# Optimization experiments

Hardware: AMD Instinct MI355X
Metric: run time of the kernel (lower is better)

The kernel has to match this reference:

```python
import jax, jax.numpy as jnp
import numpy as np

E = 8       # num experts
T = 1024    # num tokens
H = 1024    # hidden dim
I = 1024    # intermediate dim (per gate/up half)


def setup_inputs() -> dict:
    key = jax.random.key(0)
    k1, k2, k3, k4 = jax.random.split(key, 4)
    return {
        "hidden_states": jax.random.normal(k1, (T, H), jnp.float32),
        "router_logits": jax.random.normal(k2, (T, E), jnp.float32),
        # W13 stored pre-transposed as in the module: [E, H, 2*I]
        "W13": jax.random.normal(k3, (E, H, 2 * I), jnp.float32) * 0.02,
        # W2 stored pre-transposed: [E, I, H]
        "W2": jax.random.normal(k4, (E, I, H), jnp.float32) * 0.02,
        "top_k": 2,
    }


def reference(hidden_states, router_logits, W13, W2, top_k):
    num_experts = router_logits.shape[-1]
    # --- routing: topk_softmax (softmax over all experts, then top-k) ---
    probs = jax.nn.softmax(router_logits, axis=-1)            # [T, E]
    w, idx = jax.lax.top_k(probs, top_k)                      # [T, K]
    # renormalize=True path of moe_gather
    w = w / jnp.sum(w, axis=-1, keepdims=True)
    # combine weights per expert: [T, E]
    combine = jnp.sum(jax.nn.one_hot(idx, num_experts, dtype=w.dtype) * w[..., None], axis=1)
    # --- grouped gate-up GEMM + silu_and_mul ---
    h13 = jnp.einsum('th,ehf->tef', hidden_states, W13)       # [T, E, 2I]
    gate, up = jnp.split(h13, 2, axis=-1)                     # each [T, E, I]
    act = jax.nn.silu(gate) * up                              # silu_and_mul
    # --- grouped down GEMM ---
    down = jnp.einsum('tei,eih->teh', act, W2)                # [T, E, H]
    # --- combine (moe_gather) ---
    return jnp.einsum('te,teh->th', combine, down)            # [T, H]
```

## Files before the change

### kernel.cpp

```cpp
#include <hip/hip_runtime.h>
#include <hip/hip_bf16.h>
#include <stdint.h>

#define NE    8
#define NTOK  1024
#define NH    1024
#define NI    1024
#define N13   2048
#define NPAIR 2048

#define P0_ITEMS 7169
#define G1MAX    736
#define G2MAX    624

typedef __attribute__((ext_vector_type(8))) short short8;
typedef __attribute__((ext_vector_type(4))) float f32x4;
typedef unsigned short u16;
typedef unsigned int   u32;

__device__ __forceinline__ u16 f2bf(float x) {
    union { float f; u32 u; } v; v.f = x;
    return (u16)((v.u + 0x7fffu + ((v.u >> 16) & 1u)) >> 16);
}

__device__ __forceinline__ void async_ld16(u16* lds, const u16* g) {
    __builtin_amdgcn_global_load_lds(
        (const __attribute__((address_space(1))) u32*)g,
        (__attribute__((address_space(3))) u32*)lds, 16, 0, 0);
}

__device__ __forceinline__ bool find_tile(
    const int* __restrict__ counts, int tile, int bm, int ntn,
    int& e_o, int& mt_o, int& nt_o, int& cnt_o, int& base_o)
{
    int base = 0;
    #pragma unroll
    for (int e = 0; e < NE; e++) {
        const int cnt = counts[e];
        const int mtiles = (cnt + bm - 1) / bm;
        const int tiles = mtiles * ntn;
        if (tile < tiles) {
            e_o = e; mt_o = tile / ntn; nt_o = tile - (tile / ntn) * ntn;
            cnt_o = cnt; base_o = base; return true;
        }
        tile -= tiles; base += cnt;
    }
    return false;
}

__global__ __launch_bounds__(256) void prep_all_kernel(
    const float* __restrict__ X, const float* __restrict__ logits,
    const float* __restrict__ W13, const float* __restrict__ W2,
    float* __restrict__ out, int* __restrict__ counts,
    int* __restrict__ pair_tok, float* __restrict__ pair_w,
    u16* __restrict__ Xb, u16* __restrict__ W13t, u16* __restrict__ W2t)
{
    __shared__ __align__(16) float Ts[64][65];
    const int tid = threadIdx.x;
    const int b = blockIdx.x;

    if (b == 0) {
        int* s_cnt  = (int*)&Ts[0][0];
        int* s_base = s_cnt + NE;
        if (tid < NE) s_cnt[tid] = 0;
        __syncthreads();
        int eA[4][2]; int slotA[4][2]; float wA[4][2];
        #pragma unroll
        for (int i = 0; i < 4; i++) {
            const int t = tid * 4 + i;
            float l[NE];
            #pragma unroll
            for (int e = 0; e < NE; e++) l[e] = logits[t * NE + e];
            int i0 = 0;
            #pragma unroll
            for (int e = 1; e < NE; e++) if (l[e] > l[i0]) i0 = e;
            int i1 = -1;
            #pragma unroll
            for (int e = 0; e < NE; e++) {
                if (e == i0) continue;
                if (i1 < 0 || l[e] > l[i1]) i1 = e;
            }
            const float e10 = __expf(l[i1] - l[i0]);
            const float inv = 1.0f / (1.0f + e10);
            eA[i][0] = i0; eA[i][1] = i1;
            wA[i][0] = inv; wA[i][1] = e10 * inv;
            slotA[i][0] = atomicAdd(&s_cnt[i0], 1);
            slotA[i][1] = atomicAdd(&s_cnt[i1], 1);
        }
        __syncthreads();
        if (tid == 0) {
            int acc = 0;
            #pragma unroll
            for (int e = 0; e < NE; e++) { s_base[e] = acc; acc += s_cnt[e]; }
        }
        __syncthreads();
        if (tid < NE) counts[tid] = s_cnt[tid];
        #pragma unroll
        for (int i = 0; i < 4; i++) {
            const int t = tid * 4 + i;
            #pragma unroll
            for (int k = 0; k < 2; k++) {
                const int p = s_base[eA[i][k]] + slotA[i][k];
                pair_tok[p] = t;
                pair_w[p]   = wA[i][k];
            }
        }
    } else if (b <= 512) {
        const int i = (b - 1) * 256 + tid;
        const float4* s = (const float4*)X;
        const float4 a = s[2 * i], c = s[2 * i + 1];
        uint4 o;
        o.x = f2bf(a.x) | ((u32)f2bf(a.y) << 16);
        o.y = f2bf(a.z) | ((u32)f2bf(a.w) << 16);
        o.z = f2bf(c.x) | ((u32)f2bf(c.y) << 16);
        o.w = f2bf(c.z) | ((u32)f2bf(c.w) << 16);
        *(uint4*)(Xb + (size_t)i * 8) = o;
    } else if (b <= 1024) {
        const int i = ((b - 513) * 256 + tid) * 8;
        const float4 z = make_float4(0.f, 0.f, 0.f, 0.f);
        *(float4*)(out + i)     = z;
        *(float4*)(out + i + 4) = z;
    } else {
        const int wb = b - 1025;
        const float* src; u16* dst; int K, N, tb;
        if (wb < 4096) { src = W13; dst = W13t; K = NH; N = N13; tb = wb; }
        else           { src = W2;  dst = W2t;  K = NI; N = NH;  tb = wb - 4096; }
        const int ktiles = K >> 6, ntiles = N >> 6;
        const int tpe = ktiles * ntiles;
        const int e = tb / tpe;
        const int rem = tb - e * tpe;
        const int kt = rem / ntiles, nt = rem - (rem / ntiles) * ntiles;
        const float* sb = src + ((size_t)e * K + (size_t)kt * 64) * N + nt * 64;
        #pragma unroll
        for (int i = 0; i < 4; i++) {
            const int idx = tid + i * 256;
            const int r = idx >> 4, c = (idx & 15) << 2;
            const float4 v = *(const float4*)(sb + (size_t)r * N + c);
            Ts[r][c + 0] = v.x; Ts[r][c + 1] = v.y;
            Ts[r][c + 2] = v.z; Ts[r][c + 3] = v.w;
        }
        __syncthreads();
        u16* db = dst + ((size_t)e * N + (size_t)nt * 64) * K + kt * 64;
        #pragma unroll
        for (int i = 0; i < 2; i++) {
            const int u = tid + i * 256;
            const int n = u >> 3, k8 = (u & 7) << 3;
            uint4 o;
            o.x = f2bf(Ts[k8 + 0][n]) | ((u32)f2bf(Ts[k8 + 1][n]) << 16);
            o.y = f2bf(Ts[k8 + 2][n]) | ((u32)f2bf(Ts[k8 + 3][n]) << 16);
            o.z = f2bf(Ts[k8 + 4][n]) | ((u32)f2bf(Ts[k8 + 5][n]) << 16);
            o.w = f2bf(Ts[k8 + 6][n]) | ((u32)f2bf(Ts[k8 + 7][n]) << 16);
            *(uint4*)(db + (size_t)n * K + k8) = o;
        }
    }
}

__global__ __launch_bounds__(256, 2) void gemm1_kernel(
    const u16* __restrict__ Xb, const u16* __restrict__ W13t,
    const int* __restrict__ counts, const int* __restrict__ pair_tok,
    u16* __restrict__ act)
{
    int e, mt, nt, cnt, base;
    if (!find_tile(counts, blockIdx.x, 128, NI / 32, e, mt, nt, cnt, base)) return;

    __shared__ u16 As[2][128 * 32];
    __shared__ u16 Bs[2][64 * 32];

    const int tid = threadIdx.x;
    const int ct  = nt * 32;

    const int m0 = tid >> 2;
    const int sw16 = (((tid & 3) ^ (m0 & 3)) << 3);
    const int t0 = pair_tok[base + min(mt * 128 + m0, cnt - 1)];
    const int t1 = pair_tok[base + min(mt * 128 + 64 + m0, cnt - 1)];
    const u16* ga0 = Xb + (size_t)t0 * NH + sw16;
    const u16* ga1 = Xb + (size_t)t1 * NH + sw16;
    const int wcol = (m0 < 32) ? (ct + m0) : (NI + ct + m0 - 32);
    const u16* gb = W13t + ((size_t)e * N13 + wcol) * 1024 + sw16;

    const int lane = tid & 63, w = tid >> 6;
    const int quad = lane >> 4, lid = lane & 15;
    const int rw = w >> 1, cw = w & 1;
    const int fsw = (quad ^ (lid & 3)) << 3;
    int aoff[4];
    #pragma unroll
    for (int mi = 0; mi < 4; mi++)
        aoff[mi] = (rw * 64 + mi * 16 + lid) * 32 + fsw;
    const int bgoff = (cw * 16 + lid) * 32 + fsw;
    const int buoff = (32 + cw * 16 + lid) * 32 + fsw;

    f32x4 accg[4] = {};
    f32x4 accu[4] = {};

#define ISSUE1(b, k0)                                        \
    {                                                        \
        async_ld16(&As[b][tid * 8],         ga0 + (k0));     \
        async_ld16(&As[b][(tid + 256) * 8], ga1 + (k0));     \
        async_ld16(&Bs[b][tid * 8],         gb  + (k0));     \
    }
#define COMP1(b)                                                               \
    {                                                                          \
        short8 av[4];                                                          \
        _Pragma("unroll") for (int mi = 0; mi < 4; mi++)                       \
            av[mi] = *(const short8*)&As[b][aoff[mi]];                         \
        const short8 gv = *(const short8*)&Bs[b][bgoff];                       \
        const short8 uv = *(const short8*)&Bs[b][buoff];                       \
        _Pragma("unroll") for (int mi = 0; mi < 4; mi++) {                     \
            accg[mi] = __builtin_amdgcn_mfma_f32_16x16x32_bf16(                \
                av[mi], gv, accg[mi], 0, 0, 0);                                \
            accu[mi] = __builtin_amdgcn_mfma_f32_16x16x32_bf16(                \
                av[mi], uv, accu[mi], 0, 0, 0);                                \
        }                                                                      \
    }

    ISSUE1(0, 0);
    int buf = 0;
    for (int k0 = 32; k0 < NH; k0 += 32) {
        __syncthreads();
        ISSUE1(buf ^ 1, k0);
        COMP1(buf);
        buf ^= 1;
    }
    __syncthreads();
    COMP1(buf);

    const int col = ct + cw * 16 + lid;
    #pragma unroll
    for (int mi = 0; mi < 4; mi++) {
        #pragma unroll
        for (int r = 0; r < 4; r++) {
            const int row = mt * 128 + rw * 64 + mi * 16 + quad * 4 + r;
            if (row < cnt) {
                const float g = accg[mi][r], u = accu[mi][r];
                const float s = g / (1.0f + __expf(-g)) * u;
                act[(size_t)(base + row) * NI + col] = f2bf(s);
            }
        }
    }
#undef ISSUE1
#undef COMP1
}

__global__ __launch_bounds__(256, 2) void gemm2_kernel(
    const u16* __restrict__ act, const u16* __restrict__ W2t,
    const int* __restrict__ counts, const int* __restrict__ pair_tok,
    const float* __restrict__ pair_w, float* __restrict__ out)
{
    int e, mt, nt, cnt, base;
    if (!find_tile(counts, blockIdx.x, 64, NH / 64, e, mt, nt, cnt, base)) return;

    __shared__ u16 As[2][64 * 32];
    __shared__ u16 Bs[2][64 * 32];

    const int tid = threadIdx.x;
    const int ct  = nt * 64;

    const int m0 = tid >> 2;
    const int sw16 = (((tid & 3) ^ (m0 & 3)) << 3);
    const int p0 = base + min(mt * 64 + m0, cnt - 1);
    const u16* ga = act + (size_t)p0 * NI + sw16;
    const u16* gb = W2t + ((size_t)e * 1024 + ct + m0) * 1024 + sw16;

    const int lane = tid & 63, w = tid >> 6;
    const int quad = lane >> 4, lid = lane & 15;
    const int rw = w >> 1, cw = w & 1;
    const int fsw = (quad ^ (lid & 3)) << 3;
    int aoff[2], boff[2];
    #pragma unroll
    for (int mi = 0; mi < 2; mi++)
        aoff[mi] = (rw * 32 + mi * 16 + lid) * 32 + fsw;
    #pragma unroll
    for (int nj = 0; nj < 2; nj++)
        boff[nj] = (cw * 32 + nj * 16 + lid) * 32 + fsw;

    f32x4 acc[2][2] = {};

#define ISSUE2(b, k0)                                        \
    {                                                        \
        async_ld16(&As[b][tid * 8], ga + (k0));              \
        async_ld16(&Bs[b][tid * 8], gb + (k0));              \
    }
#define COMP2(b)                                                               \
    {                                                                          \
        short8 av[2], bv[2];                                                   \
        _Pragma("unroll") for (int mi = 0; mi < 2; mi++)                       \
            av[mi] = *(const short8*)&As[b][aoff[mi]];                         \
        _Pragma("unroll") for (int nj = 0; nj < 2; nj++)                       \
            bv[nj] = *(const short8*)&Bs[b][boff[nj]];                         \
        _Pragma("unroll") for (int mi = 0; mi < 2; mi++)                       \
            _Pragma("unroll") for (int nj = 0; nj < 2; nj++)                   \
                acc[mi][nj] = __builtin_amdgcn_mfma_f32_16x16x32_bf16(         \
                    av[mi], bv[nj], acc[mi][nj], 0, 0, 0);                     \
    }

    ISSUE2(0, 0);
    int buf = 0;
    for (int k0 = 32; k0 < NI; k0 += 32) {
        __syncthreads();
        ISSUE2(buf ^ 1, k0);
        COMP2(buf);
        buf ^= 1;
    }
    __syncthreads();
    COMP2(buf);

    #pragma unroll
    for (int mi = 0; mi < 2; mi++) {
        #pragma unroll
        for (int r = 0; r < 4; r++) {
            const int row = mt * 64 + rw * 32 + mi * 16 + quad * 4 + r;
            if (row < cnt) {
                const int p = base + row;
                const int t = pair_tok[p];
                const float wgt = pair_w[p];
                #pragma unroll
                for (int nj = 0; nj < 2; nj++) {
                    const int col = ct + cw * 32 + nj * 16 + lid;
                    atomicAdd(out + (size_t)t * NH + col, wgt * acc[mi][nj][r]);
                }
            }
        }
    }
#undef ISSUE2
#undef COMP2
}

extern "C" void kernel_launch(void* const* d_in, const int* in_sizes, int n_in,
                              void* d_out, int out_size, void* d_ws, size_t ws_size,
                              hipStream_t stream)
{
    const float* X      = (const float*)d_in[0];
    const float* logits = (const float*)d_in[1];
    const float* W13    = (const float*)d_in[2];
    const float* W2     = (const float*)d_in[3];
    float* out = (float*)d_out;

    char* ws = (char*)d_ws;
    int*   counts   = (int*)(ws + 0);
    int*   pair_tok = (int*)(ws + 256);
    float* pair_w   = (float*)(ws + 256 + 8192);
    u16*   Xb       = (u16*)(ws + 65536);
    u16*   W13t     = (u16*)(ws + 4194304);
    u16*   W2t      = (u16*)(ws + 4194304 + 33554432);
    u16*   act      = (u16*)(ws + 54525952);

    prep_all_kernel<<<P0_ITEMS, 256, 0, stream>>>(
        X, logits, W13, W2, out, counts, pair_tok, pair_w, Xb, W13t, W2t);
    gemm1_kernel<<<G1MAX, 256, 0, stream>>>(Xb, W13t, counts, pair_tok, act);
    gemm2_kernel<<<G2MAX, 256, 0, stream>>>(act, W2t, counts, pair_tok, pair_w, out);
}
```

Before: 178.0 us.

## Fuse W13 fp32-to-bf16 transpose into gemm1 instead of prep pass

Removes the W13 conversion/transpose blocks from the prep kernel and has gemm1 load fp32 W13 directly, packing to bf16 in registers and transposing via an LDS staging tile each k-step. This eliminates a separate 64MB read and 32MB write pass over W13. In exchange each M-tile rereads fp32 weights (twice the bytes of bf16), and B is single-buffered with an extra barrier per iteration, weakening the async pipeline.

```diff
diff --git a/kernel.cpp b/kernel.cpp
--- a/kernel.cpp
+++ b/kernel.cpp
@@ -9,7 +9,8 @@
 #define N13   2048
 #define NPAIR 2048
 
-#define P0_ITEMS 7169
+#define WT2      2048
+#define P0_ITEMS (1025 + WT2)
 #define G1MAX    736
 #define G2MAX    624
 
@@ -21,6 +22,13 @@
 __device__ __forceinline__ u16 f2bf(float x) {
     union { float f; u32 u; } v; v.f = x;
     return (u16)((v.u + 0x7fffu + ((v.u >> 16) & 1u)) >> 16);
+}
+
+__device__ __forceinline__ uint2 pack4(float4 v) {
+    uint2 o;
+    o.x = f2bf(v.x) | ((u32)f2bf(v.y) << 16);
+    o.y = f2bf(v.z) | ((u32)f2bf(v.w) << 16);
+    return o;
 }
 
 __device__ __forceinline__ void async_ld16(u16* lds, const u16* g) {
@@ -50,10 +58,10 @@
 
 __global__ __launch_bounds__(256) void prep_all_kernel(
     const float* __restrict__ X, const float* __restrict__ logits,
-    const float* __restrict__ W13, const float* __restrict__ W2,
+    const float* __restrict__ W2,
     float* __restrict__ out, int* __restrict__ counts,
     int* __restrict__ pair_tok, float* __restrict__ pair_w,
-    u16* __restrict__ Xb, u16* __restrict__ W13t, u16* __restrict__ W2t)
+    u16* __restrict__ Xb, u16* __restrict__ W2t)
 {
     __shared__ __align__(16) float Ts[64][65];
     const int tid = threadIdx.x;
@@ -121,16 +129,14 @@
         *(float4*)(out + i)     = z;
         *(float4*)(out + i + 4) = z;
     } else {
-        const int wb = b - 1025;
-        const float* src; u16* dst; int K, N, tb;
-        if (wb < 4096) { src = W13; dst = W13t; K = NH; N = N13; tb = wb; }
-        else           { src = W2;  dst = W2t;  K = NI; N = NH;  tb = wb - 4096; }
-        const int ktiles = K >> 6, ntiles = N >> 6;
-        const int tpe = ktiles * ntiles;
+        const int tb = b - 1025;
+        const int K = NI, N = NH;
+        const int ntiles = N >> 6;
+        const int tpe = (K >> 6) * ntiles;
         const int e = tb / tpe;
         const int rem = tb - e * tpe;
         const int kt = rem / ntiles, nt = rem - (rem / ntiles) * ntiles;
-        const float* sb = src + ((size_t)e * K + (size_t)kt * 64) * N + nt * 64;
+        const float* sb = W2 + ((size_t)e * K + (size_t)kt * 64) * N + nt * 64;
         #pragma unroll
         for (int i = 0; i < 4; i++) {
             const int idx = tid + i * 256;
@@ -140,7 +146,7 @@
             Ts[r][c + 2] = v.z; Ts[r][c + 3] = v.w;
         }
         __syncthreads();
-        u16* db = dst + ((size_t)e * N + (size_t)nt * 64) * K + kt * 64;
+        u16* db = W2t + ((size_t)e * N + (size_t)nt * 64) * K + kt * 64;
         #pragma unroll
         for (int i = 0; i < 2; i++) {
             const int u = tid + i * 256;
@@ -156,7 +162,7 @@
 }
 
 __global__ __launch_bounds__(256, 2) void gemm1_kernel(
-    const u16* __restrict__ Xb, const u16* __restrict__ W13t,
+    const u16* __restrict__ Xb, const float* __restrict__ W13,
     const int* __restrict__ counts, const int* __restrict__ pair_tok,
     u16* __restrict__ act)
 {
@@ -164,7 +170,8 @@
     if (!find_tile(counts, blockIdx.x, 128, NI / 32, e, mt, nt, cnt, base)) return;
 
     __shared__ u16 As[2][128 * 32];
-    __shared__ u16 Bs[2][64 * 32];
+    __shared__ u16 Lt[32][72];
+    __shared__ u16 Bs[64 * 40];
 
     const int tid = threadIdx.x;
     const int ct  = nt * 32;
@@ -175,8 +182,10 @@
     const int t1 = pair_tok[base + min(mt * 128 + 64 + m0, cnt - 1)];
     const u16* ga0 = Xb + (size_t)t0 * NH + sw16;
     const u16* ga1 = Xb + (size_t)t1 * NH + sw16;
-    const int wcol = (m0 < 32) ? (ct + m0) : (NI + ct + m0 - 32);
-    const u16* gb = W13t + ((size_t)e * N13 + wcol) * 1024 + sw16;
+
+    const int kk = tid >> 3, q = tid & 7;
+    const float* gbg = W13 + (size_t)e * NH * N13 + (size_t)kk * N13 + ct + q * 4;
+    const float* gbu = gbg + NI;
 
     const int lane = tid & 63, w = tid >> 6;
     const int quad = lane >> 4, lid = lane & 15;
@@ -186,25 +195,26 @@
     #pragma unroll
     for (int mi = 0; mi < 4; mi++)
         aoff[mi] = (rw * 64 + mi * 16 + lid) * 32 + fsw;
-    const int bgoff = (cw * 16 + lid) * 32 + fsw;
-    const int buoff = (32 + cw * 16 + lid) * 32 + fsw;
+    const int bgoff = (cw * 16 + lid) * 40 + quad * 8;
+    const int buoff = (32 + cw * 16 + lid) * 40 + quad * 8;
+
+    const int gn = tid >> 2, gk8 = (tid & 3) << 3;
 
     f32x4 accg[4] = {};
     f32x4 accu[4] = {};
 
-#define ISSUE1(b, k0)                                        \
-    {                                                        \
-        async_ld16(&As[b][tid * 8],         ga0 + (k0));     \
-        async_ld16(&As[b][(tid + 256) * 8], ga1 + (k0));     \
-        async_ld16(&Bs[b][tid * 8],         gb  + (k0));     \
+#define ISSUE_A(b, k0)                                        \
+    {                                                         \
+        async_ld16(&As[b][tid * 8],         ga0 + (k0));      \
+        async_ld16(&As[b][(tid + 256) * 8], ga1 + (k0));      \
     }
 #define COMP1(b)                                                               \
     {                                                                          \
         short8 av[4];                                                          \
         _Pragma("unroll") for (int mi = 0; mi < 4; mi++)                       \
             av[mi] = *(const short8*)&As[b][aoff[mi]];                         \
-        const short8 gv = *(const short8*)&Bs[b][bgoff];                       \
-        const short8 uv = *(const short8*)&Bs[b][buoff];                       \
+        const short8 gv = *(const short8*)&Bs[bgoff];                          \
+        const short8 uv = *(const short8*)&Bs[buoff];                          \
         _Pragma("unroll") for (int mi = 0; mi < 4; mi++) {                     \
             accg[mi] = __builtin_amdgcn_mfma_f32_16x16x32_bf16(                \
                 av[mi], gv, accg[mi], 0, 0, 0);                                \
@@ -213,16 +223,33 @@
         }                                                                      \
     }
 
-    ISSUE1(0, 0);
+    float4 bg = *(const float4*)gbg;
+    float4 bu = *(const float4*)gbu;
+    ISSUE_A(0, 0);
     int buf = 0;
-    for (int k0 = 32; k0 < NH; k0 += 32) {
-        __syncthreads();
-        ISSUE1(buf ^ 1, k0);
+
+    for (int k0 = 0; k0 < NH; k0 += 32) {
+        *(uint2*)&Lt[kk][q * 4]      = pack4(bg);
+        *(uint2*)&Lt[kk][32 + q * 4] = pack4(bu);
+        const bool nxt = (k0 + 32) < NH;
+        __syncthreads();
+        if (nxt) {
+            ISSUE_A(buf ^ 1, k0 + 32);
+            bg = *(const float4*)(gbg + (size_t)(k0 + 32) * N13);
+            bu = *(const float4*)(gbu + (size_t)(k0 + 32) * N13);
+        }
+        {
+            uint4 o;
+            o.x = Lt[gk8 + 0][gn] | ((u32)Lt[gk8 + 1][gn] << 16);
+            o.y = Lt[gk8 + 2][gn] | ((u32)Lt[gk8 + 3][gn] << 16);
+            o.z = Lt[gk8 + 4][gn] | ((u32)Lt[gk8 + 5][gn] << 16);
+            o.w = Lt[gk8 + 6][gn] | ((u32)Lt[gk8 + 7][gn] << 16);
+            *(uint4*)&Bs[gn * 40 + gk8] = o;
+        }
+        __syncthreads();
         COMP1(buf);
         buf ^= 1;
     }
-    __syncthreads();
-    COMP1(buf);
 
     const int col = ct + cw * 16 + lid;
     #pragma unroll
@@ -237,7 +264,7 @@
             }
         }
     }
-#undef ISSUE1
+#undef ISSUE_A
 #undef COMP1
 }
 
@@ -340,12 +367,11 @@
     int*   pair_tok = (int*)(ws + 256);
     float* pair_w   = (float*)(ws + 256 + 8192);
     u16*   Xb       = (u16*)(ws + 65536);
-    u16*   W13t     = (u16*)(ws + 4194304);
     u16*   W2t      = (u16*)(ws + 4194304 + 33554432);
     u16*   act      = (u16*)(ws + 54525952);
 
     prep_all_kernel<<<P0_ITEMS, 256, 0, stream>>>(
-        X, logits, W13, W2, out, counts, pair_tok, pair_w, Xb, W13t, W2t);
-    gemm1_kernel<<<G1MAX, 256, 0, stream>>>(Xb, W13t, counts, pair_tok, act);
+        X, logits, W2, out, counts, pair_tok, pair_w, Xb, W2t);
+    gemm1_kernel<<<G1MAX, 256, 0, stream>>>(Xb, W13, counts, pair_tok, act);
     gemm2_kernel<<<G2MAX, 256, 0, stream>>>(act, W2t, counts, pair_tok, pair_w, out);
 }
```

Result: slower. 184.3 us (+3.5%).
